# Kernel tuning notes

Hardware: AMD Instinct MI355X
Metric: run time of the kernel (lower is better)

## Reference

```python
import jax, jax.numpy as jnp
import numpy as np


def setup_inputs() -> dict:
    key = jax.random.key(0)
    ks = jax.random.split(key, 6)
    B, L, N, C, D = 8, 512, 2048, 1024, 128
    return {
        "teacher_logits": jax.random.normal(ks[0], (B, L, N), dtype=jnp.float32),
        "teacher_features": jax.random.normal(ks[1], (B, N, C), dtype=jnp.float32),
        "Wq": jax.random.normal(ks[2], (D, C), dtype=jnp.float32) * (1.0 / np.sqrt(C)),
        "bq": jnp.zeros((D,), dtype=jnp.float32),
        "Wk": jax.random.normal(ks[3], (D, C), dtype=jnp.float32) * (1.0 / np.sqrt(C)),
        "bk": jnp.zeros((D,), dtype=jnp.float32),
    }


def reference(teacher_logits, teacher_features, Wq, bq, Wk, bk):
    # Linear projections (torch nn.Linear: x @ W^T + b)
    query = jnp.einsum("bnc,dc->bnd", teacher_features, Wq) + bq  # [B,N,D]
    key = jnp.einsum("bnc,dc->bnd", teacher_features, Wk) + bk    # [B,N,D]
    energy = jnp.einsum("bnd,bmd->bnm", query, key)               # [B,N,N]
    attention = jax.nn.softmax(energy, axis=-1)                   # softmax over last dim
    # x_m = teacher_logits @ attention^T : [B,L,N] x [B,N,N]^T -> [B,L,N]
    x_m = jnp.einsum("bln,bmn->blm", teacher_logits, attention)
    return x_m
```

## Files before the change

### kernel.cpp

```cpp
#include <hip/hip_runtime.h>
#include <hip/hip_bf16.h>

#define B_ 8
#define L_ 512
#define N_ 2048
#define C_ 1024
#define D_ 128

typedef __attribute__((ext_vector_type(8))) short    short8;
typedef __attribute__((ext_vector_type(8))) _Float16 half8;
typedef __attribute__((ext_vector_type(4))) float    floatx4;

static __device__ __forceinline__ float s2f(short s) {
    return __uint_as_float(((unsigned)(unsigned short)s) << 16);
}
static __device__ __forceinline__ short f2bf(float f) {
    union { __hip_bfloat16 h; short s; } u;
    u.h = __float2bfloat16(f);
    return u.s;
}

struct F8 { float v[8]; };

static __device__ __forceinline__ F8 load8(const void* raw, long off, int is_bf16) {
    F8 r;
    if (is_bf16) {
        short8 x = *reinterpret_cast<const short8*>((const short*)raw + off);
        #pragma unroll
        for (int i = 0; i < 8; ++i) r.v[i] = s2f(x[i]);
    } else {
        const float* p = (const float*)raw + off;
        float4 a = *reinterpret_cast<const float4*>(p);
        float4 b = *reinterpret_cast<const float4*>(p + 4);
        r.v[0]=a.x; r.v[1]=a.y; r.v[2]=a.z; r.v[3]=a.w;
        r.v[4]=b.x; r.v[5]=b.y; r.v[6]=b.z; r.v[7]=b.w;
    }
    return r;
}

static __device__ __forceinline__ float bias_at(const void* raw, int d, int is_bf16) {
    return is_bf16 ? s2f(((const short*)raw)[d]) : ((const float*)raw)[d];
}

static __device__ __forceinline__ void load_lds16(const void* g, void* l) {
    __builtin_amdgcn_global_load_lds(
        (const __attribute__((address_space(1))) void*)g,
        (__attribute__((address_space(3))) void*)l, 16, 0, 0);
}

__global__ void detect_kernel(const unsigned* __restrict__ words, int* __restrict__ flag) {
    int cnt = 0;
    for (int i = threadIdx.x; i < 256; i += 64) {
        float lowv = __uint_as_float(words[i] << 16);
        float a = fabsf(lowv);
        if (a >= 1e-5f && a <= 100.0f) cnt++;
    }
    #pragma unroll
    for (int off = 32; off; off >>= 1) cnt += __shfl_down(cnt, off);
    if (threadIdx.x == 0) flag[0] = (cnt > 128) ? 1 : 0;
}

__global__ __launch_bounds__(1024) void zero_kernel(float* __restrict__ Z, int n) {
    int i = blockIdx.x * 1024 + threadIdx.x;
    if (i < n) Z[i] = 0.0f;
}

__global__ __launch_bounds__(256) void cvt_kernel(const void* __restrict__ in_raw,
                                                  short* __restrict__ out, long n,
                                                  const int* __restrict__ flag) {
    if (*flag) return;
    long i = ((long)blockIdx.x * 256 + threadIdx.x) * 8;
    if (i >= n) return;
    F8 x = load8(in_raw, i, 0);
    short8 o;
    #pragma unroll
    for (int j = 0; j < 8; ++j) o[j] = f2bf(x.v[j]);
    *reinterpret_cast<short8*>(out + i) = o;
}

__global__ __launch_bounds__(256) void cvt_half_kernel(const void* __restrict__ in_raw,
                                                       _Float16* __restrict__ out, long n,
                                                       const int* __restrict__ flag) {
    if (*flag) return;
    long i = ((long)blockIdx.x * 256 + threadIdx.x) * 8;
    if (i >= n) return;
    F8 x = load8(in_raw, i, 0);
    half8 o;
    #pragma unroll
    for (int j = 0; j < 8; ++j) o[j] = (_Float16)x.v[j];
    *reinterpret_cast<half8*>(out + i) = o;
}

__global__ __launch_bounds__(256) void proj_kernel(
    const void* __restrict__ Fraw,
    const void* __restrict__ Wq_raw, const void* __restrict__ Wk_raw,
    const _Float16* __restrict__ Wq_h, const _Float16* __restrict__ Wk_h,
    const void* __restrict__ bq_raw, const void* __restrict__ bk_raw,
    _Float16* __restrict__ Q, _Float16* __restrict__ K,
    const int* __restrict__ flag)
{
    const int is_bf16 = *flag;
    const int tid  = threadIdx.x;
    const int wave = tid >> 6;
    const int lane = tid & 63;
    const int quad = lane >> 4;
    const int l16  = lane & 15;
    const long r0  = (long)blockIdx.x * 64;

    const bool isK = (blockIdx.y != 0);
    const void* braw = isK ? bk_raw : bq_raw;
    _Float16* Out    = isK ? K : Q;

    const int m0 = (wave & 1) * 32;
    const int n0 = (wave >> 1) * 64;

    __shared__ short Ft[64 * 32];
    __shared__ short Wt[128 * 32];

    floatx4 acc[2][4] = {};

    const int srow  = lane >> 2;
    const int skoff = (lane & 3) * 8;

    if (is_bf16) {
        const short* Fr = (const short*)Fraw;
        const short* Wr = (const short*)(isK ? Wk_raw : Wq_raw);
        for (int kb = 0; kb < 32; ++kb) {
            const int k0 = kb * 32;
            load_lds16(Fr + (r0 + wave * 16 + srow) * (long)C_ + k0 + skoff,
                       Ft + wave * 512 + lane * 8);
            #pragma unroll
            for (int jj = 0; jj < 2; ++jj) {
                load_lds16(Wr + (long)(wave * 32 + jj * 16 + srow) * C_ + k0 + skoff,
                           Wt + (wave * 2 + jj) * 512 + lane * 8);
            }
            __syncthreads();

            short8 af[2], bfr[4];
            #pragma unroll
            for (int t = 0; t < 2; ++t)
                af[t] = *reinterpret_cast<const short8*>(Ft + (m0 + t * 16 + l16) * 32 + quad * 8);
            #pragma unroll
            for (int u = 0; u < 4; ++u)
                bfr[u] = *reinterpret_cast<const short8*>(Wt + (n0 + u * 16 + l16) * 32 + quad * 8);
            #pragma unroll
            for (int t = 0; t < 2; ++t)
                #pragma unroll
                for (int u = 0; u < 4; ++u)
                    acc[t][u] = __builtin_amdgcn_mfma_f32_16x16x32_bf16(af[t], bfr[u], acc[t][u], 0, 0, 0);
            __syncthreads();
        }
    } else {
        const _Float16* Wh = isK ? Wk_h : Wq_h;
        _Float16* Fth = (_Float16*)Ft;
        _Float16* Wth = (_Float16*)Wt;
        for (int kb = 0; kb < 32; ++kb) {
            const int k0 = kb * 32;
            #pragma unroll
            for (int jj = 0; jj < 2; ++jj) {
                load_lds16(Wh + (long)(wave * 32 + jj * 16 + srow) * C_ + k0 + skoff,
                           Wth + (wave * 2 + jj) * 512 + lane * 8);
            }
            {
                F8 x = load8(Fraw, (r0 + (tid >> 2)) * (long)C_ + k0 + (tid & 3) * 8, 0);
                half8 h;
                #pragma unroll
                for (int j = 0; j < 8; ++j) h[j] = (_Float16)x.v[j];
                *reinterpret_cast<half8*>(Fth + tid * 8) = h;
            }
            __syncthreads();

            half8 af[2], bfr[4];
            #pragma unroll
            for (int t = 0; t < 2; ++t)
                af[t] = *reinterpret_cast<const half8*>(Fth + (m0 + t * 16 + l16) * 32 + quad * 8);
            #pragma unroll
            for (int u = 0; u < 4; ++u)
                bfr[u] = *reinterpret_cast<const half8*>(Wth + (n0 + u * 16 + l16) * 32 + quad * 8);
            #pragma unroll
            for (int t = 0; t < 2; ++t)
                #pragma unroll
                for (int u = 0; u < 4; ++u)
                    acc[t][u] = __builtin_amdgcn_mfma_f32_16x16x32_f16(af[t], bfr[u], acc[t][u], 0, 0, 0);
            __syncthreads();
        }
    }

    #pragma unroll
    for (int u = 0; u < 4; ++u) {
        const int d = n0 + u * 16 + l16;
        const float bv = bias_at(braw, d, is_bf16);
        #pragma unroll
        for (int t = 0; t < 2; ++t)
            #pragma unroll
            for (int r = 0; r < 4; ++r) {
                const long row = r0 + m0 + t * 16 + quad * 4 + r;
                Out[row * D_ + d] = (_Float16)(acc[t][u][r] + bv);
            }
    }
}

__global__ __launch_bounds__(512) void attn_pz_kernel(
    const _Float16* __restrict__ Q,
    const _Float16* __restrict__ K,
    short* __restrict__ P,
    float* __restrict__ Z)
{
    const int b    = blockIdx.y;
    const int i0   = blockIdx.x * 32;
    const int wave = threadIdx.x >> 6;
    const int lane = threadIdx.x & 63;
    const int quad = lane >> 4;
    const int l16  = lane & 15;

    const _Float16* Qb = Q + (long)b * N_ * D_;
    const _Float16* Kb = K + (long)b * N_ * D_;

    half8 a[2][4];
    #pragma unroll
    for (int v = 0; v < 2; ++v)
        #pragma unroll
        for (int s = 0; s < 4; ++s)
            a[v][s] = *reinterpret_cast<const half8*>(
                Qb + (long)(i0 + v * 16 + l16) * D_ + s * 32 + quad * 8);

    const int jbase = wave * 256;
    short* Pb = P + (long)b * N_ * N_;

    float zpart[2][4] = {};

    #pragma unroll
    for (int t = 0; t < 16; ++t) {
        const _Float16* krow = Kb + (long)(jbase + t * 16 + l16) * D_ + quad * 8;
        floatx4 acc[2] = {};
        #pragma unroll
        for (int s = 0; s < 4; ++s) {
            half8 kf = *reinterpret_cast<const half8*>(krow + s * 32);
            acc[0] = __builtin_amdgcn_mfma_f32_16x16x32_f16(a[0][s], kf, acc[0], 0, 0, 0);
            acc[1] = __builtin_amdgcn_mfma_f32_16x16x32_f16(a[1][s], kf, acc[1], 0, 0, 0);
        }
        const int j = jbase + t * 16 + l16;
        #pragma unroll
        for (int v = 0; v < 2; ++v)
            #pragma unroll
            for (int r = 0; r < 4; ++r) {
                float e = __expf(acc[v][r]);
                zpart[v][r] += e;
                Pb[(long)(i0 + v * 16 + quad * 4 + r) * N_ + j] = f2bf(e);
            }
    }

    #pragma unroll
    for (int v = 0; v < 2; ++v)
        #pragma unroll
        for (int r = 0; r < 4; ++r) {
            float z = zpart[v][r];
            z += __shfl_xor(z, 1);
            z += __shfl_xor(z, 2);
            z += __shfl_xor(z, 4);
            z += __shfl_xor(z, 8);
            if (l16 == 0)
                atomicAdd(&Z[(long)b * N_ + i0 + v * 16 + quad * 4 + r], z);
        }
}

__global__ __launch_bounds__(256) void xm_kernel(
    const void* __restrict__ Lraw,
    const short* __restrict__ Lcvt,
    const short* __restrict__ A,
    const float* __restrict__ Z,
    void* __restrict__ OutRaw,
    const int* __restrict__ flag)
{
    const int is_bf16 = *flag;
    const int b  = blockIdx.z;
    const int r0 = blockIdx.x * 128;
    const int c0 = blockIdx.y * 128;
    const int wave = threadIdx.x >> 6;
    const int lane = threadIdx.x & 63;
    const int quad = lane >> 4;
    const int l16  = lane & 15;

    __shared__ short Atile[128 * 64];
    __shared__ short Btile[128 * 64];

    const short* Lb = (is_bf16 ? (const short*)Lraw : Lcvt) + (long)b * L_ * N_;
    const short* Ab = A + (long)b * N_ * N_;

    const int m0 = (wave & 1) * 64;
    const int n0 = (wave >> 1) * 64;

    floatx4 acc[4][4] = {};

    const int srow  = lane >> 3;
    const int skoff = (lane & 7) * 8;

    for (int kb = 0; kb < 32; ++kb) {
        const int k0 = kb * 64;
        #pragma unroll
        for (int j = 0; j < 8; ++j) {
            const int cc = wave * 8 + j;
            if (cc < 16) {
                const short* src = Lb + (long)(r0 + cc * 8 + srow) * N_ + k0 + skoff;
                load_lds16(src, Atile + cc * 512);
            } else {
                const int c8 = cc - 16;
                const short* src = Ab + (long)(c0 + c8 * 8 + srow) * N_ + k0 + skoff;
                load_lds16(src, Btile + c8 * 512);
            }
        }
        __syncthreads();

        #pragma unroll
        for (int ks = 0; ks < 2; ++ks) {
            short8 af[4], bf[4];
            #pragma unroll
            for (int t = 0; t < 4; ++t)
                af[t] = *reinterpret_cast<const short8*>(
                    Atile + (m0 + t * 16 + l16) * 64 + ks * 32 + quad * 8);
            #pragma unroll
            for (int u = 0; u < 4; ++u)
                bf[u] = *reinterpret_cast<const short8*>(
                    Btile + (n0 + u * 16 + l16) * 64 + ks * 32 + quad * 8);
            #pragma unroll
            for (int t = 0; t < 4; ++t)
                #pragma unroll
                for (int u = 0; u < 4; ++u)
                    acc[t][u] = __builtin_amdgcn_mfma_f32_16x16x32_bf16(af[t], bf[u], acc[t][u], 0, 0, 0);
        }
        __syncthreads();
    }

    float invz[4];
    #pragma unroll
    for (int u = 0; u < 4; ++u)
        invz[u] = 1.0f / Z[(long)b * N_ + c0 + n0 + u * 16 + l16];

    if (is_bf16) {
        short* Ob = (short*)OutRaw + (long)b * L_ * N_;
        #pragma unroll
        for (int t = 0; t < 4; ++t)
            #pragma unroll
            for (int u = 0; u < 4; ++u)
                #pragma unroll
                for (int r = 0; r < 4; ++r) {
                    const long row = r0 + m0 + t * 16 + quad * 4 + r;
                    const int  col = c0 + n0 + u * 16 + l16;
                    Ob[row * N_ + col] = f2bf(acc[t][u][r] * invz[u]);
                }
    } else {
        float* Ob = (float*)OutRaw + (long)b * L_ * N_;
        #pragma unroll
        for (int t = 0; t < 4; ++t)
            #pragma unroll
            for (int u = 0; u < 4; ++u)
                #pragma unroll
                for (int r = 0; r < 4; ++r) {
                    const long row = r0 + m0 + t * 16 + quad * 4 + r;
                    const int  col = c0 + n0 + u * 16 + l16;
                    Ob[row * N_ + col] = acc[t][u][r] * invz[u];
                }
    }
}

extern "C" void kernel_launch(void* const* d_in, const int* in_sizes, int n_in,
                              void* d_out, int out_size, void* d_ws, size_t ws_size,
                              hipStream_t stream) {
    const void* logits_raw = d_in[0];
    const void* feats_raw  = d_in[1];
    const void* wq_raw     = d_in[2];
    const void* bq_raw     = d_in[3];
    const void* wk_raw     = d_in[4];
    const void* bk_raw     = d_in[5];

    char* ws = (char*)d_ws;
    size_t off = 0;
    int* flag = (int*)(ws + off);           off += 256;
    short* logb = (short*)(ws + off);       off += (size_t)B_ * L_ * N_ * 2;
    _Float16* Wq_h = (_Float16*)(ws + off); off += (size_t)D_ * C_ * 2;
    _Float16* Wk_h = (_Float16*)(ws + off); off += (size_t)D_ * C_ * 2;
    _Float16* Q = (_Float16*)(ws + off);    off += (size_t)B_ * N_ * D_ * 2;
    _Float16* K = (_Float16*)(ws + off);    off += (size_t)B_ * N_ * D_ * 2;
    float* Z = (float*)(ws + off);          off += (size_t)B_ * N_ * 4;
    short* A = (short*)(ws + off);          off += (size_t)B_ * N_ * N_ * 2;

    hipLaunchKernelGGL(detect_kernel, dim3(1), dim3(64), 0, stream,
                       (const unsigned*)feats_raw, flag);
    hipLaunchKernelGGL(zero_kernel, dim3((B_ * N_ + 1023) / 1024), dim3(1024), 0, stream,
                       Z, B_ * N_);
    hipLaunchKernelGGL(cvt_kernel, dim3((B_ * L_ * N_) / (256 * 8)), dim3(256), 0, stream,
                       logits_raw, logb, (long)B_ * L_ * N_, flag);
    hipLaunchKernelGGL(cvt_half_kernel, dim3((D_ * C_) / (256 * 8)), dim3(256), 0, stream,
                       wq_raw, Wq_h, (long)D_ * C_, flag);
    hipLaunchKernelGGL(cvt_half_kernel, dim3((D_ * C_) / (256 * 8)), dim3(256), 0, stream,
                       wk_raw, Wk_h, (long)D_ * C_, flag);
    hipLaunchKernelGGL(proj_kernel, dim3(B_ * N_ / 64, 2), dim3(256), 0, stream,
                       feats_raw, wq_raw, wk_raw, Wq_h, Wk_h, bq_raw, bk_raw, Q, K, flag);
    hipLaunchKernelGGL(attn_pz_kernel, dim3(N_ / 32, B_), dim3(512), 0, stream,
                       Q, K, A, Z);
    hipLaunchKernelGGL(xm_kernel, dim3(L_ / 128, N_ / 128, B_), dim3(256), 0, stream,
                       logits_raw, logb, A, Z, d_out, flag);
}
```

Before: 274.2 us.

## Fuse Q/K projection into one block and XOR-swizzle LDS tiles

The projection kernel now computes Q and K together in one 512-thread block, so each features tile is loaded once and shared by both weight matrices instead of being reloaded by two separate grid rows. LDS tiles in both the projection and the x_m GEMM kernels are stored with an XOR swizzle on the 16-byte chunk index, meant to remove bank conflicts on the MFMA operand reads. The cost is extra index arithmetic and a larger block with half its waves idle during the feature load.

After: 266.3 us. 2.9% less time.

```diff
diff --git a/kernel.cpp b/kernel.cpp
--- a/kernel.cpp
+++ b/kernel.cpp
@@ -91,7 +91,7 @@
     *reinterpret_cast<half8*>(out + i) = o;
 }
 
-__global__ __launch_bounds__(256) void proj_kernel(
+__global__ __launch_bounds__(512) void proj_kernel(
     const void* __restrict__ Fraw,
     const void* __restrict__ Wq_raw, const void* __restrict__ Wk_raw,
     const _Float16* __restrict__ Wq_h, const _Float16* __restrict__ Wk_h,
@@ -107,42 +107,51 @@
     const int l16  = lane & 15;
     const long r0  = (long)blockIdx.x * 64;
 
-    const bool isK = (blockIdx.y != 0);
-    const void* braw = isK ? bk_raw : bq_raw;
-    _Float16* Out    = isK ? K : Q;
-
-    const int m0 = (wave & 1) * 32;
-    const int n0 = (wave >> 1) * 64;
+    const int m0   = (wave & 1) * 32;
+    const int col0 = (wave >> 1) * 64;
 
     __shared__ short Ft[64 * 32];
-    __shared__ short Wt[128 * 32];
+    __shared__ short Wt[256 * 32];
 
     floatx4 acc[2][4] = {};
 
-    const int srow  = lane >> 2;
-    const int skoff = (lane & 3) * 8;
+    const int srow = lane >> 2;
+    const int sg   = (lane & 3) ^ ((srow >> 1) & 3);
+    const int skoff = sg * 8;
 
     if (is_bf16) {
-        const short* Fr = (const short*)Fraw;
-        const short* Wr = (const short*)(isK ? Wk_raw : Wq_raw);
+        const short* Fr  = (const short*)Fraw;
+        const short* Wqr = (const short*)Wq_raw;
+        const short* Wkr = (const short*)Wk_raw;
         for (int kb = 0; kb < 32; ++kb) {
             const int k0 = kb * 32;
-            load_lds16(Fr + (r0 + wave * 16 + srow) * (long)C_ + k0 + skoff,
-                       Ft + wave * 512 + lane * 8);
             #pragma unroll
             for (int jj = 0; jj < 2; ++jj) {
-                load_lds16(Wr + (long)(wave * 32 + jj * 16 + srow) * C_ + k0 + skoff,
-                           Wt + (wave * 2 + jj) * 512 + lane * 8);
+                const int c = wave * 2 + jj;
+                const short* Wr = (c < 8) ? Wqr : Wkr;
+                const int wrow = (c & 7) * 16 + srow;
+                load_lds16(Wr + (long)wrow * C_ + k0 + skoff,
+                           Wt + c * 512 + lane * 8);
+            }
+            if (wave < 4) {
+                load_lds16(Fr + (r0 + wave * 16 + srow) * (long)C_ + k0 + skoff,
+                           Ft + wave * 512 + lane * 8);
             }
             __syncthreads();
 
             short8 af[2], bfr[4];
             #pragma unroll
-            for (int t = 0; t < 2; ++t)
-                af[t] = *reinterpret_cast<const short8*>(Ft + (m0 + t * 16 + l16) * 32 + quad * 8);
-            #pragma unroll
-            for (int u = 0; u < 4; ++u)
-                bfr[u] = *reinterpret_cast<const short8*>(Wt + (n0 + u * 16 + l16) * 32 + quad * 8);
+            for (int t = 0; t < 2; ++t) {
+                const int row = m0 + t * 16 + l16;
+                const int ph  = quad ^ ((row >> 1) & 3);
+                af[t] = *reinterpret_cast<const short8*>(Ft + row * 32 + ph * 8);
+            }
+            #pragma unroll
+            for (int u = 0; u < 4; ++u) {
+                const int wrow = col0 + u * 16 + l16;
+                const int ph   = quad ^ ((wrow >> 1) & 3);
+                bfr[u] = *reinterpret_cast<const short8*>(Wt + wrow * 32 + ph * 8);
+            }
             #pragma unroll
             for (int t = 0; t < 2; ++t)
                 #pragma unroll
@@ -151,18 +160,22 @@
             __syncthreads();
         }
     } else {
-        const _Float16* Wh = isK ? Wk_h : Wq_h;
         _Float16* Fth = (_Float16*)Ft;
         _Float16* Wth = (_Float16*)Wt;
         for (int kb = 0; kb < 32; ++kb) {
             const int k0 = kb * 32;
             #pragma unroll
             for (int jj = 0; jj < 2; ++jj) {
-                load_lds16(Wh + (long)(wave * 32 + jj * 16 + srow) * C_ + k0 + skoff,
-                           Wth + (wave * 2 + jj) * 512 + lane * 8);
-            }
-            {
-                F8 x = load8(Fraw, (r0 + (tid >> 2)) * (long)C_ + k0 + (tid & 3) * 8, 0);
+                const int c = wave * 2 + jj;
+                const _Float16* Wh = (c < 8) ? Wq_h : Wk_h;
+                const int wrow = (c & 7) * 16 + srow;
+                load_lds16(Wh + (long)wrow * C_ + k0 + skoff,
+                           Wth + c * 512 + lane * 8);
+            }
+            if (tid < 256) {
+                const int frow = tid >> 2;
+                const int fg   = (tid & 3) ^ ((frow >> 1) & 3);
+                F8 x = load8(Fraw, (r0 + frow) * (long)C_ + k0 + fg * 8, 0);
                 half8 h;
                 #pragma unroll
                 for (int j = 0; j < 8; ++j) h[j] = (_Float16)x.v[j];
@@ -172,11 +185,17 @@
 
             half8 af[2], bfr[4];
             #pragma unroll
-            for (int t = 0; t < 2; ++t)
-                af[t] = *reinterpret_cast<const half8*>(Fth + (m0 + t * 16 + l16) * 32 + quad * 8);
-            #pragma unroll
-            for (int u = 0; u < 4; ++u)
-                bfr[u] = *reinterpret_cast<const half8*>(Wth + (n0 + u * 16 + l16) * 32 + quad * 8);
+            for (int t = 0; t < 2; ++t) {
+                const int row = m0 + t * 16 + l16;
+                const int ph  = quad ^ ((row >> 1) & 3);
+                af[t] = *reinterpret_cast<const half8*>(Fth + row * 32 + ph * 8);
+            }
+            #pragma unroll
+            for (int u = 0; u < 4; ++u) {
+                const int wrow = col0 + u * 16 + l16;
+                const int ph   = quad ^ ((wrow >> 1) & 3);
+                bfr[u] = *reinterpret_cast<const half8*>(Wth + wrow * 32 + ph * 8);
+            }
             #pragma unroll
             for (int t = 0; t < 2; ++t)
                 #pragma unroll
@@ -186,9 +205,12 @@
         }
     }
 
+    const bool isK = (col0 >= 128);
+    const void* braw = isK ? bk_raw : bq_raw;
+    _Float16* Out    = isK ? K : Q;
     #pragma unroll
     for (int u = 0; u < 4; ++u) {
-        const int d = n0 + u * 16 + l16;
+        const int d = (col0 + u * 16 + l16) & 127;
         const float bv = bias_at(braw, d, is_bf16);
         #pragma unroll
         for (int t = 0; t < 2; ++t)
@@ -293,7 +315,7 @@
     floatx4 acc[4][4] = {};
 
     const int srow  = lane >> 3;
-    const int skoff = (lane & 7) * 8;
+    const int skoff = ((lane & 7) ^ srow) * 8;
 
     for (int kb = 0; kb < 32; ++kb) {
         const int k0 = kb * 64;
@@ -315,13 +337,17 @@
         for (int ks = 0; ks < 2; ++ks) {
             short8 af[4], bf[4];
             #pragma unroll
-            for (int t = 0; t < 4; ++t)
-                af[t] = *reinterpret_cast<const short8*>(
-                    Atile + (m0 + t * 16 + l16) * 64 + ks * 32 + quad * 8);
-            #pragma unroll
-            for (int u = 0; u < 4; ++u)
-                bf[u] = *reinterpret_cast<const short8*>(
-                    Btile + (n0 + u * 16 + l16) * 64 + ks * 32 + quad * 8);
+            for (int t = 0; t < 4; ++t) {
+                const int row = m0 + t * 16 + l16;
+                const int ph  = (ks * 4 + quad) ^ (row & 7);
+                af[t] = *reinterpret_cast<const short8*>(Atile + row * 64 + ph * 8);
+            }
+            #pragma unroll
+            for (int u = 0; u < 4; ++u) {
+                const int row = n0 + u * 16 + l16;
+                const int ph  = (ks * 4 + quad) ^ (row & 7);
+                bf[u] = *reinterpret_cast<const short8*>(Btile + row * 64 + ph * 8);
+            }
             #pragma unroll
             for (int t = 0; t < 4; ++t)
                 #pragma unroll
@@ -394,7 +420,7 @@
                        wq_raw, Wq_h, (long)D_ * C_, flag);
     hipLaunchKernelGGL(cvt_half_kernel, dim3((D_ * C_) / (256 * 8)), dim3(256), 0, stream,
                        wk_raw, Wk_h, (long)D_ * C_, flag);
-    hipLaunchKernelGGL(proj_kernel, dim3(B_ * N_ / 64, 2), dim3(256), 0, stream,
+    hipLaunchKernelGGL(proj_kernel, dim3(B_ * N_ / 64), dim3(512), 0, stream,
                        feats_raw, wq_raw, wk_raw, Wq_h, Wk_h, bq_raw, bk_raw, Q, K, flag);
     hipLaunchKernelGGL(attn_pz_kernel, dim3(N_ / 32, B_), dim3(512), 0, stream,
                        Q, K, A, Z);
```
